# Performance work log

Hardware: AMD Instinct MI355X
Metric: run time of the kernel (lower is better)

The kernel has to match this reference:

```python
import jax, jax.numpy as jnp
import numpy as np

NUM_NODES = 100000
EMBED_DIM = 128
HIDDEN_DIM = 128
NUM_EDGES = 600000
NUM_LABELS = 200000


def setup_inputs() -> dict:
    key = jax.random.key(0)
    ks = jax.random.split(key, 12)
    edge_index = jax.random.randint(ks[0], (2, NUM_EDGES), 0, NUM_NODES)
    edge_label_index = jax.random.randint(ks[1], (2, NUM_LABELS), 0, NUM_NODES)
    s = 0.05
    return {
        "edge_index": edge_index,
        "edge_label_index": edge_label_index,
        "emb": jax.random.normal(ks[2], (NUM_NODES, EMBED_DIM), jnp.float32) * s,
        # conv1: lin_l (aggregated neighbors, with bias), lin_r (root, no bias)
        "W1l": jax.random.normal(ks[3], (EMBED_DIM, HIDDEN_DIM), jnp.float32) * s,
        "b1": jnp.zeros((HIDDEN_DIM,), jnp.float32),
        "W1r": jax.random.normal(ks[4], (EMBED_DIM, HIDDEN_DIM), jnp.float32) * s,
        # conv2
        "W2l": jax.random.normal(ks[5], (HIDDEN_DIM, HIDDEN_DIM), jnp.float32) * s,
        "b2": jnp.zeros((HIDDEN_DIM,), jnp.float32),
        "W2r": jax.random.normal(ks[6], (HIDDEN_DIM, HIDDEN_DIM), jnp.float32) * s,
        # final link predictor Linear(2*hidden, 1)
        "Wlin": jax.random.normal(ks[7], (2 * HIDDEN_DIM, 1), jnp.float32) * s,
        "blin": jnp.zeros((1,), jnp.float32),
    }


def _sage_conv(x, src, dst, Wl, bl, Wr):
    # mean aggregation of source-node features at destination nodes
    n = x.shape[0]
    msg_sum = jax.ops.segment_sum(x[src], dst, num_segments=n)  # [N, d]
    cnt = jax.ops.segment_sum(jnp.ones_like(src, dtype=x.dtype), dst, num_segments=n)
    agg = msg_sum / jnp.maximum(cnt, 1.0)[:, None]
    return agg @ Wl + bl + x @ Wr


def reference(edge_index, edge_label_index, emb, W1l, b1, W1r, W2l, b2, W2r, Wlin, blin):
    src, dst = edge_index[0], edge_index[1]
    x = jax.nn.relu(_sage_conv(emb, src, dst, W1l, b1, W1r))
    x = _sage_conv(x, src, dst, W2l, b2, W2r)
    s, d = edge_label_index[0], edge_label_index[1]
    pair = jnp.concatenate([x[s], x[d]], axis=1)  # [L, 2*hidden]
    return (pair @ Wlin + blin).reshape(-1)
```

## Files before the change

### kernel.cpp

```cpp
#include <hip/hip_runtime.h>
#include <hip/hip_bf16.h>

#define N_NODES 100000
#define N_EDGES 600000
#define N_LABELS 200000
#define DIM 128
#define NPARTS 391
#define NT_TILES 6250
#define FG_GRID 2048

using short8 = __attribute__((ext_vector_type(8))) short;
using f32x2  = __attribute__((ext_vector_type(2))) float;
using f32x4  = __attribute__((ext_vector_type(4))) float;
using u32x2  = __attribute__((ext_vector_type(2))) unsigned;
using u32x4  = __attribute__((ext_vector_type(4))) unsigned;

__device__ __forceinline__ float b2f(short s) {
    union { unsigned u; float f; } c;
    c.u = ((unsigned)(unsigned short)s) << 16;
    return c.f;
}
__device__ __forceinline__ f32x2 b2f2(unsigned u) {
    union { unsigned u; float f; } lo, hi;
    lo.u = u << 16;
    hi.u = u & 0xffff0000u;
    f32x2 r; r[0] = lo.f; r[1] = hi.f;
    return r;
}
__device__ __forceinline__ short f2b(float f) {
    __hip_bfloat16 h = __float2bfloat16(f);
    return *reinterpret_cast<short*>(&h);
}
__device__ __forceinline__ unsigned f2b2u(float x, float y) {
    __hip_bfloat162 h = __float22bfloat162_rn(make_float2(x, y));
    return *reinterpret_cast<unsigned*>(&h);
}

__global__ void prep_k(const float* __restrict__ W1l, const float* __restrict__ W1r,
                       short* __restrict__ BT1,
                       const float* __restrict__ W2l, const float* __restrict__ W2r,
                       const float* __restrict__ Wlin, const float* __restrict__ b2,
                       float* __restrict__ up, float* __restrict__ uq,
                       float* __restrict__ vp, float* __restrict__ vq,
                       float2* __restrict__ cpq, int* __restrict__ cnt) {
    int b = blockIdx.x;
    int t = threadIdx.x;
    if (b < 128) {
        int i = b * 256 + t;
        int n = i >> 7, k = i & 127;
        float v = (n < 128) ? W1l[k * 128 + n] : W1r[k * 128 + (n - 128)];
        BT1[n * 128 + k] = f2b(v);
    } else if (b == 128) {
        const float* W = (t < 128) ? W2l : W2r;
        int k = t & 127;
        float s0 = 0.f, s1 = 0.f;
        for (int n = 0; n < 128; ++n) {
            float w = W[k * 128 + n];
            s0 += w * Wlin[n];
            s1 += w * Wlin[128 + n];
        }
        if (t < 128) { up[k] = s0; uq[k] = s1; }
        else         { vp[k] = s0; vq[k] = s1; }
    } else if (b == 129) {
        if (t < 64) {
            float p0 = b2[t] * Wlin[t] + b2[t + 64] * Wlin[t + 64];
            float q0 = b2[t] * Wlin[128 + t] + b2[t + 64] * Wlin[192 + t];
#pragma unroll
            for (int m = 1; m <= 32; m <<= 1) {
                p0 += __shfl_xor(p0, m, 64);
                q0 += __shfl_xor(q0, m, 64);
            }
            if (t == 0) *cpq = make_float2(p0, q0);
        }
    } else {
        int i = (b - 130) * 256 + t;
        if (i < N_NODES) cnt[i] = 0;
    }
}

__global__ void count_k(const int* __restrict__ ei, int* __restrict__ cnt,
                        int* __restrict__ rank) {
    int e = blockIdx.x * blockDim.x + threadIdx.x;
    if (e < N_EDGES) rank[e] = atomicAdd(&cnt[ei[N_EDGES + e]], 1);
}

__global__ void scan1_k(const int* __restrict__ cnt, int* __restrict__ rowptr,
                        int* __restrict__ partials) {
    __shared__ int s[256];
    int t = threadIdx.x;
    int i = blockIdx.x * 256 + t;
    int v = (i < N_NODES) ? cnt[i] : 0;
    s[t] = v;
    __syncthreads();
    for (int off = 1; off < 256; off <<= 1) {
        int x = s[t];
        int y = (t >= off) ? s[t - off] : 0;
        __syncthreads();
        s[t] = x + y;
        __syncthreads();
    }
    if (i < N_NODES) rowptr[i] = s[t] - v;
    if (t == 255) partials[blockIdx.x] = s[255];
}

__global__ void scanB_k(const int* __restrict__ partials, int* __restrict__ rowptr) {
    __shared__ int s[512];
    __shared__ int base_s;
    int t = threadIdx.x;
    int v = (t < NPARTS) ? partials[t] : 0;
    s[t] = v;
    __syncthreads();
    for (int off = 1; off < 512; off <<= 1) {
        int x = s[t];
        int y = (t >= off) ? s[t - off] : 0;
        __syncthreads();
        s[t] = x + y;
        __syncthreads();
    }
    int b = blockIdx.x;
    if (t == 0) base_s = (b > 0) ? s[b - 1] : 0;
    if (b == 0 && t == 0) rowptr[N_NODES] = s[NPARTS - 1];
    __syncthreads();
    if (t < 256) {
        int i = b * 256 + t;
        if (i < N_NODES) rowptr[i] += base_s;
    }
}

__global__ __launch_bounds__(256, 4) void fillgemm_k(const int* __restrict__ ei,
                                                     const int* __restrict__ rank,
                                                     const int* __restrict__ rowptr,
                                                     int* __restrict__ adj,
                                                     const float* __restrict__ Af,
                                                     const short* __restrict__ BT,
                                                     short* __restrict__ Hl,
                                                     short* __restrict__ Hr) {
    for (int e = blockIdx.x * 256 + threadIdx.x; e < N_EDGES; e += FG_GRID * 256) {
        int d = ei[N_EDGES + e];
        adj[rowptr[d] + rank[e]] = ei[e];
    }

    int lane = threadIdx.x & 63;
    int wave = threadIdx.x >> 6;
    int quad = lane >> 4;
    int l16  = lane & 15;
    short* __restrict__ H = (wave < 2) ? Hl : Hr;
    int fbase = (wave & 1) * 64;

    short8 Wf[4][4];
#pragma unroll
    for (int t = 0; t < 4; ++t)
#pragma unroll
        for (int kk = 0; kk < 4; ++kk)
            Wf[t][kk] = *(const short8*)(BT + (wave * 64 + t * 16 + l16) * DIM + kk * 32 + quad * 8);

    for (int s = blockIdx.x; s < NT_TILES; s += FG_GRID) {
        long arow = (long)s * 16 + l16;
        short8 xf[4];
#pragma unroll
        for (int kk = 0; kk < 4; ++kk) {
            f32x4 a0 = *(const f32x4*)(Af + arow * DIM + kk * 32 + quad * 8);
            f32x4 a1 = *(const f32x4*)(Af + arow * DIM + kk * 32 + quad * 8 + 4);
            unsigned* xu = (unsigned*)&xf[kk];
            xu[0] = f2b2u(a0[0], a0[1]);
            xu[1] = f2b2u(a0[2], a0[3]);
            xu[2] = f2b2u(a1[0], a1[1]);
            xu[3] = f2b2u(a1[2], a1[3]);
        }
        f32x4 acc[4];
#pragma unroll
        for (int t = 0; t < 4; ++t)
#pragma unroll
            for (int r = 0; r < 4; ++r) acc[t][r] = 0.f;
#pragma unroll
        for (int kk = 0; kk < 4; ++kk)
#pragma unroll
            for (int t = 0; t < 4; ++t)
                acc[t] = __builtin_amdgcn_mfma_f32_16x16x32_bf16(Wf[t][kk], xf[kk], acc[t], 0, 0, 0);
#pragma unroll
        for (int t = 0; t < 4; ++t) {
            u32x2 o;
            o[0] = f2b2u(acc[t][0], acc[t][1]);
            o[1] = f2b2u(acc[t][2], acc[t][3]);
            *(u32x2*)(H + arow * DIM + fbase + t * 16 + quad * 4) = o;
        }
    }
}

__device__ __forceinline__ void gather_mean(const short* __restrict__ Hl,
                                            const int* __restrict__ rowptr,
                                            const int* __restrict__ adj,
                                            int node, int lane, f32x2 sum[4], float& inv) {
    int g  = lane >> 4;
    int f0 = (lane & 15) << 3;
    int beg = rowptr[node];
    int deg = rowptr[node + 1] - beg;
#pragma unroll
    for (int d = 0; d < 4; ++d) { sum[d][0] = 0.f; sum[d][1] = 0.f; }

    int av = (lane < deg) ? adj[beg + lane] : 0;
    int degc = deg < 64 ? deg : 64;

    u32x4 h0;
    bool v0 = false;
    if (degc > 0) {
        int idx = __shfl(av, g, 64);
        v0 = g < degc;
        if (v0) h0 = *(const u32x4*)(Hl + (long)idx * DIM + f0);
    }
    for (int e0 = 4; e0 < degc; e0 += 4) {
        int idx = __shfl(av, e0 + g, 64);
        bool v1 = (e0 + g) < degc;
        u32x4 h1;
        if (v1) h1 = *(const u32x4*)(Hl + (long)idx * DIM + f0);
        if (v0) {
#pragma unroll
            for (int d = 0; d < 4; ++d) sum[d] += b2f2(h0[d]);
        }
        h0 = h1; v0 = v1;
    }
    if (v0) {
#pragma unroll
        for (int d = 0; d < 4; ++d) sum[d] += b2f2(h0[d]);
    }
    for (int e0 = 64; e0 < deg; e0 += 4) {
        int e = e0 + g;
        if (e < deg) {
            int idx = adj[beg + e];
            u32x4 h = *(const u32x4*)(Hl + (long)idx * DIM + f0);
#pragma unroll
            for (int d = 0; d < 4; ++d) sum[d] += b2f2(h[d]);
        }
    }
#pragma unroll
    for (int d = 0; d < 4; ++d)
#pragma unroll
        for (int c = 0; c < 2; ++c) {
            sum[d][c] += __shfl_xor(sum[d][c], 16, 64);
            sum[d][c] += __shfl_xor(sum[d][c], 32, 64);
        }
    inv = deg > 0 ? 1.f / (float)deg : 0.f;
}

__global__ void agg1_k(const short* __restrict__ Hl, const short* __restrict__ Hr,
                       const int* __restrict__ rowptr, const int* __restrict__ adj,
                       const float* __restrict__ b1,
                       const float* __restrict__ up, const float* __restrict__ uq,
                       const float* __restrict__ vp, const float* __restrict__ vq,
                       float2* __restrict__ S, float2* __restrict__ T) {
    int lane = threadIdx.x & 63;
    int node = blockIdx.x * 4 + (threadIdx.x >> 6);
    int f0 = (lane & 15) << 3;
    if (node >= N_NODES) return;

    f32x2 sum[4]; float inv;
    gather_mean(Hl, rowptr, adj, node, lane, sum, inv);

    u32x4 hru = *(const u32x4*)(Hr + (long)node * DIM + f0);
    f32x2 x2[4];
#pragma unroll
    for (int d = 0; d < 4; ++d) {
        f32x2 hr2 = b2f2(hru[d]);
        f32x2 bb  = *(const f32x2*)(b1 + f0 + 2 * d);
        f32x2 v   = sum[d] * inv + hr2 + bb;
        x2[d][0] = fmaxf(v[0], 0.f);
        x2[d][1] = fmaxf(v[1], 0.f);
    }

    f32x2 ap2 = {0.f, 0.f}, aq2 = {0.f, 0.f}, tp2 = {0.f, 0.f}, tq2 = {0.f, 0.f};
#pragma unroll
    for (int d = 0; d < 4; ++d) {
        f32x2 u0 = *(const f32x2*)(up + f0 + 2 * d);
        f32x2 u1 = *(const f32x2*)(uq + f0 + 2 * d);
        f32x2 w0 = *(const f32x2*)(vp + f0 + 2 * d);
        f32x2 w1 = *(const f32x2*)(vq + f0 + 2 * d);
        ap2 += x2[d] * u0;
        aq2 += x2[d] * u1;
        tp2 += x2[d] * w0;
        tq2 += x2[d] * w1;
    }
    float ap = ap2[0] + ap2[1], aq = aq2[0] + aq2[1];
    float tp = tp2[0] + tp2[1], tq = tq2[0] + tq2[1];
#pragma unroll
    for (int m = 1; m <= 8; m <<= 1) {
        ap += __shfl_xor(ap, m, 64);
        aq += __shfl_xor(aq, m, 64);
        tp += __shfl_xor(tp, m, 64);
        tq += __shfl_xor(tq, m, 64);
    }
    if (lane == 0) {
        S[node] = make_float2(ap, aq);
        T[node] = make_float2(tp, tq);
    }
}

__global__ void agg2_k(const int* __restrict__ rowptr, const int* __restrict__ adj,
                       const float2* __restrict__ S, const float2* __restrict__ T,
                       const float2* __restrict__ cpq,
                       float* __restrict__ p, float* __restrict__ q) {
    int lane = threadIdx.x & 63;
    int wavei = blockIdx.x * 4 + (threadIdx.x >> 6);
    int slot = lane & 3;
    int node = wavei * 16 + (lane >> 2);
    if (node >= N_NODES) return;
    int beg = rowptr[node], end = rowptr[node + 1];
    float sp = 0.f, sq = 0.f;
    for (int e = beg + slot; e < end; e += 4) {
        float2 v = S[adj[e]];
        sp += v.x; sq += v.y;
    }
    sp += __shfl_xor(sp, 1, 64); sp += __shfl_xor(sp, 2, 64);
    sq += __shfl_xor(sq, 1, 64); sq += __shfl_xor(sq, 2, 64);
    if (slot == 0) {
        int deg = end - beg;
        float inv = deg > 0 ? 1.f / (float)deg : 0.f;
        float2 t = T[node];
        float2 c = *cpq;
        p[node] = sp * inv + t.x + c.x;
        q[node] = sq * inv + t.y + c.y;
    }
}

__global__ void out_k(const int* __restrict__ eli, const float* __restrict__ p,
                      const float* __restrict__ q, const float* __restrict__ blin,
                      float* __restrict__ out) {
    int i = blockIdx.x * blockDim.x + threadIdx.x;
    if (i < N_LABELS) out[i] = p[eli[i]] + q[eli[N_LABELS + i]] + blin[0];
}


extern "C" void kernel_launch(void* const* d_in, const int* in_sizes, int n_in,
                              void* d_out, int out_size, void* d_ws, size_t ws_size,
                              hipStream_t stream) {
    const int*   edge_index = (const int*)d_in[0];
    const int*   eli        = (const int*)d_in[1];
    const float* emb        = (const float*)d_in[2];
    const float* W1l        = (const float*)d_in[3];
    const float* b1         = (const float*)d_in[4];
    const float* W1r        = (const float*)d_in[5];
    const float* W2l        = (const float*)d_in[6];
    const float* b2         = (const float*)d_in[7];
    const float* W2r        = (const float*)d_in[8];
    const float* Wlin       = (const float*)d_in[9];
    const float* blin       = (const float*)d_in[10];
    float* out = (float*)d_out;

    char* ws = (char*)d_ws;
    size_t off = 0;
    auto alloc = [&](size_t bytes) -> void* {
        off = (off + 255) & ~(size_t)255;
        void* ptr = ws + off;
        off += bytes;
        return ptr;
    };

    short* Hl  = (short*)alloc((size_t)N_NODES * DIM * 2);
    short* Hr  = (short*)alloc((size_t)N_NODES * DIM * 2);
    short* BT1 = (short*)alloc(256 * 128 * 2);
    float* up = (float*)alloc(128 * 4);
    float* uq = (float*)alloc(128 * 4);
    float* vp = (float*)alloc(128 * 4);
    float* vq = (float*)alloc(128 * 4);
    float2* cpq = (float2*)alloc(8);
    int* cnt      = (int*)alloc((size_t)N_NODES * 4);
    int* rowptr   = (int*)alloc((size_t)(N_NODES + 1) * 4);
    int* rank     = (int*)alloc((size_t)N_EDGES * 4);
    int* adj      = (int*)alloc((size_t)N_EDGES * 4);
    int* partials = (int*)alloc(NPARTS * 4);
    float2* S     = (float2*)alloc((size_t)N_NODES * 8);
    float2* T     = (float2*)alloc((size_t)N_NODES * 8);
    float* p      = (float*)alloc((size_t)N_NODES * 4);
    float* q      = (float*)alloc((size_t)N_NODES * 4);

    prep_k<<<130 + NPARTS, 256, 0, stream>>>(W1l, W1r, BT1, W2l, W2r, Wlin, b2,
                                             up, uq, vp, vq, cpq, cnt);
    count_k<<<(N_EDGES + 255) / 256, 256, 0, stream>>>(edge_index, cnt, rank);
    scan1_k<<<NPARTS, 256, 0, stream>>>(cnt, rowptr, partials);
    scanB_k<<<NPARTS, 512, 0, stream>>>(partials, rowptr);

    fillgemm_k<<<FG_GRID, 256, 0, stream>>>(edge_index, rank, rowptr, adj, emb, BT1, Hl, Hr);

    agg1_k<<<N_NODES / 4, 256, 0, stream>>>(Hl, Hr, rowptr, adj, b1, up, uq, vp, vq, S, T);

    agg2_k<<<(N_NODES + 63) / 64, 256, 0, stream>>>(rowptr, adj, S, T, cpq, p, q);
    out_k<<<(N_LABELS + 255) / 256, 256, 0, stream>>>(eli, p, q, blin, out);
}
```

Baseline: 258.1 us.

## Stage 64-row A tiles and GEMM outputs through LDS for coalesced access

The fused fill+GEMM kernel now processes 64-row tiles per block. The fp32 input rows are loaded cooperatively, converted to bf16 and staged in padded LDS. MFMA results are also staged in LDS so that Hl and Hr are written with full 16-byte coalesced row stores instead of scattered 8-byte fragments. The grid is smaller and occupancy drops from 4 to 3 blocks per CU, which adds LDS traffic and barriers in exchange for better global memory coalescing.

Result: faster. 233.2 us (-9.6%).

```diff
diff --git a/kernel.cpp b/kernel.cpp
--- a/kernel.cpp
+++ b/kernel.cpp
@@ -6,8 +6,11 @@
 #define N_LABELS 200000
 #define DIM 128
 #define NPARTS 391
-#define NT_TILES 6250
-#define FG_GRID 2048
+#define MT 64
+#define NMT 1563
+#define FG_GRID 768
+#define LDA 136
+#define LDC 280
 
 using short8 = __attribute__((ext_vector_type(8))) short;
 using f32x2  = __attribute__((ext_vector_type(2))) float;
@@ -127,7 +130,7 @@
     }
 }
 
-__global__ __launch_bounds__(256, 4) void fillgemm_k(const int* __restrict__ ei,
+__global__ __launch_bounds__(256, 3) void fillgemm_k(const int* __restrict__ ei,
                                                      const int* __restrict__ rank,
                                                      const int* __restrict__ rowptr,
                                                      int* __restrict__ adj,
@@ -135,17 +138,19 @@
                                                      const short* __restrict__ BT,
                                                      short* __restrict__ Hl,
                                                      short* __restrict__ Hr) {
-    for (int e = blockIdx.x * 256 + threadIdx.x; e < N_EDGES; e += FG_GRID * 256) {
+    __shared__ short lA[MT * LDA];
+    __shared__ short lC[MT * LDC];
+    int tid = threadIdx.x;
+
+    for (int e = blockIdx.x * 256 + tid; e < N_EDGES; e += FG_GRID * 256) {
         int d = ei[N_EDGES + e];
         adj[rowptr[d] + rank[e]] = ei[e];
     }
 
-    int lane = threadIdx.x & 63;
-    int wave = threadIdx.x >> 6;
+    int lane = tid & 63;
+    int wave = tid >> 6;
     int quad = lane >> 4;
     int l16  = lane & 15;
-    short* __restrict__ H = (wave < 2) ? Hl : Hr;
-    int fbase = (wave & 1) * 64;
 
     short8 Wf[4][4];
 #pragma unroll
@@ -154,35 +159,67 @@
         for (int kk = 0; kk < 4; ++kk)
             Wf[t][kk] = *(const short8*)(BT + (wave * 64 + t * 16 + l16) * DIM + kk * 32 + quad * 8);
 
-    for (int s = blockIdx.x; s < NT_TILES; s += FG_GRID) {
-        long arow = (long)s * 16 + l16;
-        short8 xf[4];
-#pragma unroll
-        for (int kk = 0; kk < 4; ++kk) {
-            f32x4 a0 = *(const f32x4*)(Af + arow * DIM + kk * 32 + quad * 8);
-            f32x4 a1 = *(const f32x4*)(Af + arow * DIM + kk * 32 + quad * 8 + 4);
-            unsigned* xu = (unsigned*)&xf[kk];
-            xu[0] = f2b2u(a0[0], a0[1]);
-            xu[1] = f2b2u(a0[2], a0[3]);
-            xu[2] = f2b2u(a1[0], a1[1]);
-            xu[3] = f2b2u(a1[2], a1[3]);
-        }
-        f32x4 acc[4];
-#pragma unroll
-        for (int t = 0; t < 4; ++t)
-#pragma unroll
-            for (int r = 0; r < 4; ++r) acc[t][r] = 0.f;
-#pragma unroll
-        for (int kk = 0; kk < 4; ++kk)
+    for (int mt = blockIdx.x; mt < NMT; mt += FG_GRID) {
+        long base = (long)mt * MT;
+
+        __syncthreads();
+#pragma unroll
+        for (int i = 0; i < 8; ++i) {
+            int c = tid + i * 256;
+            int row = c >> 5;
+            int k4 = (c & 31) << 2;
+            long grow = base + row;
+            f32x4 a;
+            if (grow < N_NODES) a = *(const f32x4*)(Af + grow * DIM + k4);
+            else { a[0] = 0.f; a[1] = 0.f; a[2] = 0.f; a[3] = 0.f; }
+            u32x2 o;
+            o[0] = f2b2u(a[0], a[1]);
+            o[1] = f2b2u(a[2], a[3]);
+            *(u32x2*)(lA + row * LDA + k4) = o;
+        }
+        __syncthreads();
+
+#pragma unroll
+        for (int sub = 0; sub < 4; ++sub) {
+            int r0 = sub * 16;
+            short8 xf[4];
+#pragma unroll
+            for (int kk = 0; kk < 4; ++kk)
+                xf[kk] = *(const short8*)(lA + (r0 + l16) * LDA + kk * 32 + quad * 8);
+            f32x4 acc[4];
 #pragma unroll
             for (int t = 0; t < 4; ++t)
-                acc[t] = __builtin_amdgcn_mfma_f32_16x16x32_bf16(Wf[t][kk], xf[kk], acc[t], 0, 0, 0);
-#pragma unroll
-        for (int t = 0; t < 4; ++t) {
-            u32x2 o;
-            o[0] = f2b2u(acc[t][0], acc[t][1]);
-            o[1] = f2b2u(acc[t][2], acc[t][3]);
-            *(u32x2*)(H + arow * DIM + fbase + t * 16 + quad * 4) = o;
+#pragma unroll
+                for (int r = 0; r < 4; ++r) acc[t][r] = 0.f;
+#pragma unroll
+            for (int kk = 0; kk < 4; ++kk)
+#pragma unroll
+                for (int t = 0; t < 4; ++t)
+                    acc[t] = __builtin_amdgcn_mfma_f32_16x16x32_bf16(Wf[t][kk], xf[kk], acc[t], 0, 0, 0);
+#pragma unroll
+            for (int t = 0; t < 4; ++t) {
+                u32x2 o;
+                o[0] = f2b2u(acc[t][0], acc[t][1]);
+                o[1] = f2b2u(acc[t][2], acc[t][3]);
+                *(u32x2*)(lC + (r0 + l16) * LDC + wave * 64 + t * 16 + quad * 4) = o;
+            }
+        }
+        __syncthreads();
+
+#pragma unroll
+        for (int half = 0; half < 2; ++half) {
+            short* __restrict__ H = half ? Hr : Hl;
+#pragma unroll
+            for (int i = 0; i < 4; ++i) {
+                int c2 = tid + i * 256;
+                int row = c2 >> 4;
+                int f8 = (c2 & 15) << 3;
+                long grow = base + row;
+                if (grow < N_NODES) {
+                    short8 v = *(const short8*)(lC + row * LDC + half * 128 + f8);
+                    *(short8*)(H + grow * DIM + f8) = v;
+                }
+            }
         }
     }
 }
```
